# Performance work log

Hardware: AMD Instinct MI355X
Metric: run time of the kernel (lower is better)

Reference implementation:

```python
import jax, jax.numpy as jnp
import numpy as np

B, N, C, H, D = 1, 256, 128, 4, 32  # batch, n_res, c_z, heads, head_dim
LN_EPS = 1e-5


def setup_inputs() -> dict:
    key = jax.random.key(0)
    ks = jax.random.split(key, 10)
    s = 0.02
    return {
        "act": jax.random.normal(ks[0], (B, N, N, C), dtype=jnp.float32),
        "mask": jnp.ones((B, N, N), dtype=jnp.float32),
        "ln_g": jnp.ones((C,), dtype=jnp.float32),
        "ln_b": jnp.zeros((C,), dtype=jnp.float32),
        "w2d": jax.random.normal(ks[1], (C, H), dtype=jnp.float32) * s,
        "wq": jax.random.normal(ks[2], (C, H, D), dtype=jnp.float32) * s,
        "wk": jax.random.normal(ks[3], (C, H, D), dtype=jnp.float32) * s,
        "wv": jax.random.normal(ks[4], (C, H, D), dtype=jnp.float32) * s,
        "wg": jax.random.normal(ks[5], (C, H, D), dtype=jnp.float32) * s,
        "bg": jnp.ones((H, D), dtype=jnp.float32),
        "wo": jax.random.normal(ks[6], (H, D, C), dtype=jnp.float32) * s,
        "bo": jnp.zeros((C,), dtype=jnp.float32),
    }


def reference(act, mask, ln_g, ln_b, w2d, wq, wk, wv, wg, bg, wo, bo):
    # LayerNorm over channel dim
    mu = jnp.mean(act, axis=-1, keepdims=True)
    var = jnp.mean(jnp.square(act - mu), axis=-1, keepdims=True)
    x = (act - mu) * jax.lax.rsqrt(var + LN_EPS) * ln_g + ln_b  # [B,N,N,C]

    # mask bias: [B, I, 1, 1, K]
    mask_bias = (1e9 * (mask - 1.0))[:, :, None, None, :]
    # nonbatched pair bias: [B, 1, H, Q, K]
    nb_bias = jnp.einsum('bqkc,ch->bhqk', x, w2d)[:, None]

    scale = 1.0 / jnp.sqrt(jnp.asarray(D, dtype=x.dtype))
    q = jnp.einsum('bijc,chd->bijhd', x, wq) * scale  # [B,I,Q,H,D]
    k = jnp.einsum('bijc,chd->bijhd', x, wk)
    v = jnp.einsum('bijc,chd->bijhd', x, wv)

    logits = jnp.einsum('biqhd,bikhd->bihqk', q, k) + mask_bias + nb_bias
    a = jax.nn.softmax(logits, axis=-1)  # [B,I,H,Q,K]
    o = jnp.einsum('bihqk,bikhd->biqhd', a, v)  # [B,I,Q,H,D]

    g = jax.nn.sigmoid(jnp.einsum('bijc,chd->bijhd', x, wg) + bg)
    o = o * g
    out = jnp.einsum('biqhd,hdc->biqc', o, wo) + bo  # [B,N,N,C]
    return out
```

## Files before the change

kernel.cpp:

```cpp
#include <hip/hip_runtime.h>

#define QK_SCALE 0.17677669529663689f

typedef float f4 __attribute__((ext_vector_type(4)));
typedef short bf16x8 __attribute__((ext_vector_type(8)));
typedef float f32x4 __attribute__((ext_vector_type(4)));
typedef unsigned short us4 __attribute__((ext_vector_type(4)));

__device__ __forceinline__ unsigned short f2bf(float x){
  unsigned int u = __float_as_uint(x);
  u += 0x7fffu + ((u >> 16) & 1u);
  return (unsigned short)(u >> 16);
}
__device__ __forceinline__ float bf2f(unsigned short h){
  return __uint_as_float(((unsigned int)h) << 16);
}
__device__ __forceinline__ f32x4 mfma16(bf16x8 a, bf16x8 b, f32x4 c){
  return __builtin_amdgcn_mfma_f32_16x16x32_bf16(a, b, c, 0, 0, 0);
}
__device__ __forceinline__ void gload_lds16(const void* g, void* s){
  __builtin_amdgcn_global_load_lds(
      (const __attribute__((address_space(1))) unsigned int*)g,
      (__attribute__((address_space(3))) unsigned int*)s, 16, 0, 0);
}

__global__ __launch_bounds__(256)
void k_prep(const float* __restrict__ wq, const float* __restrict__ wk,
            const float* __restrict__ wv, const float* __restrict__ wg,
            const float* __restrict__ wo, unsigned short* __restrict__ pk)
{
  const int m = blockIdx.x;
  const float* W = (m==0)? wq : (m==1)? wk : (m==2)? wv : (m==3)? wg : wo;
  const float scale = (m==0)? QK_SCALE : 1.0f;
  unsigned short* dst = pk + (long)m * 32768;
  for (int ent = threadIdx.x; ent < 2048; ent += 256){
    const int l = ent & 63, ktn = ent >> 6;
    const int kt = ktn & 3, nt = ktn >> 2;
    unsigned short* ph = dst + ((nt*4 + kt)*2 + 0)*512 + l*8;
    unsigned short* pl = dst + ((nt*4 + kt)*2 + 1)*512 + l*8;
    #pragma unroll
    for (int e = 0; e < 8; ++e){
      const int row = kt*32 + (l>>4)*8 + e;
      const int col = nt*16 + (l&15);
      float v = W[row*128 + col] * scale;
      unsigned short hh = f2bf(v);
      ph[e] = hh;
      pl[e] = f2bf(v - bf2f(hh));
    }
  }
}

__global__ __launch_bounds__(512, 2)
void k_proj(const float* __restrict__ act, const float* __restrict__ ln_g,
            const float* __restrict__ ln_b, const float* __restrict__ w2d,
            const unsigned short* __restrict__ pk, const float* __restrict__ bg,
            unsigned short* __restrict__ qf, unsigned short* __restrict__ kf,
            unsigned short* __restrict__ vt, unsigned short* __restrict__ gg,
            float* __restrict__ b2d)
{
  __shared__ float xs[128*132];
  __shared__ unsigned short afr[8*4*2*512];
  __shared__ unsigned short sc[8*640];
  const int t = threadIdx.x, w = t>>6, l = t&63, g16 = l>>4, c = l&15;
  const long p0 = (long)blockIdx.x * 128;
  const int bi = (int)(p0 >> 8);
  const int qb0 = (int)(p0 & 255);

  { const f4* af = (const f4*)(act + p0*128);
    #pragma unroll
    for (int j = 0; j < 8; ++j){
      int fi = t + j*512, r = fi>>5, c4 = (fi&31)<<2;
      *(f4*)&xs[r*132 + c4] = af[fi];
    } }
  __syncthreads();
  {
    const int r = t>>2, sub = t&3;
    float s=0.f, s2=0.f;
    #pragma unroll 8
    for (int jj=0; jj<32; ++jj){ float x = xs[r*132+sub*32+jj]; s+=x; s2+=x*x; }
    s += __shfl_xor(s,1); s2 += __shfl_xor(s2,1);
    s += __shfl_xor(s,2); s2 += __shfl_xor(s2,2);
    const float mu = s*(1.f/128.f);
    const float iv = rsqrtf(fmaxf(s2*(1.f/128.f)-mu*mu,0.f)+1e-5f);
    #pragma unroll 8
    for (int jj=0; jj<32; ++jj){
      int cc = sub*32+jj;
      xs[r*132+cc] = (xs[r*132+cc]-mu)*iv*ln_g[cc]+ln_b[cc];
    } }
  __syncthreads();

  #pragma unroll
  for (int kt = 0; kt < 4; ++kt){
    const float* xp = &xs[(w*16+c)*132 + kt*32 + g16*8];
    f4 x0 = *(const f4*)xp, x1 = *(const f4*)(xp+4);
    bf16x8 hv, lv;
    #pragma unroll
    for (int e = 0; e < 8; ++e){
      float vvv = (e<4)? x0[e] : x1[e-4];
      unsigned short hh = f2bf(vvv);
      hv[e] = (short)hh; lv[e] = (short)f2bf(vvv - bf2f(hh));
    }
    *(bf16x8*)&afr[((w*4+kt)*2+0)*512 + l*8] = hv;
    *(bf16x8*)&afr[((w*4+kt)*2+1)*512 + l*8] = lv;
  }
  {
    const int r = t>>2, hh = t&3;
    float s = 0.f;
    #pragma unroll 8
    for (int cc = 0; cc < 128; ++cc) s += xs[r*132+cc]*w2d[cc*4+hh];
    b2d[hh*65536 + (int)p0 + r] = s;
  }
  __syncthreads();

  unsigned short* scw = sc + w*640;

  #pragma unroll
  for (int pass = 0; pass < 2; ++pass){
    bf16x8 bh0[4], bl0[4], bh1[4], bl1[4];
    { const int ntg = w*4 + pass*2;
      #pragma unroll
      for (int kt = 0; kt < 4; ++kt){
        bh0[kt] = *(const bf16x8*)(pk + ((ntg*4+kt)*2+0)*512 + l*8);
        bl0[kt] = *(const bf16x8*)(pk + ((ntg*4+kt)*2+1)*512 + l*8);
        bh1[kt] = *(const bf16x8*)(pk + (((ntg+1)*4+kt)*2+0)*512 + l*8);
        bl1[kt] = *(const bf16x8*)(pk + (((ntg+1)*4+kt)*2+1)*512 + l*8);
      } }
    for (int rt = 0; rt < 8; ++rt){
      bf16x8 ah[4], al[4];
      #pragma unroll
      for (int kt = 0; kt < 4; ++kt){
        ah[kt] = *(const bf16x8*)&afr[((rt*4+kt)*2+0)*512 + l*8];
        al[kt] = *(const bf16x8*)&afr[((rt*4+kt)*2+1)*512 + l*8];
      }
      f32x4 a0 = {0.f,0.f,0.f,0.f}, a1 = {0.f,0.f,0.f,0.f};
      #pragma unroll
      for (int kt = 0; kt < 4; ++kt){
        a0 = mfma16(ah[kt], bh0[kt], a0);
        a1 = mfma16(ah[kt], bh1[kt], a1);
        a0 = mfma16(ah[kt], bl0[kt], a0);
        a1 = mfma16(ah[kt], bl1[kt], a1);
        a0 = mfma16(al[kt], bh0[kt], a0);
        a1 = mfma16(al[kt], bh1[kt], a1);
      }
      if (w < 4){
        #pragma unroll
        for (int j = 0; j < 4; ++j){
          scw[(g16*4+j)*40 + c]      = f2bf(a0[j]);
          scw[(g16*4+j)*40 + 16 + c] = f2bf(a1[j]);
        }
        asm volatile("" ::: "memory");
        bf16x8 fr = *(const bf16x8*)&scw[c*40 + g16*8];
        const int head = (w&1)*2 + pass;
        unsigned short* dst = (w < 2) ? qf : kf;
        *(bf16x8*)&dst[(((long)bi*4+head)*16 + (qb0>>4) + rt)*512 + l*8] = fr;
        asm volatile("" ::: "memory");
      } else if (w < 6){
        const int ntv0 = (w-4)*4 + pass*2;
        const int kv = qb0 + rt*16 + g16*4;
        #pragma unroll
        for (int np = 0; np < 2; ++np){
          const int colg = (ntv0+np)*16 + c;
          const int head = colg >> 5, d = colg & 31;
          f32x4 aa = np ? a1 : a0;
          us4 v4;
          #pragma unroll
          for (int j = 0; j < 4; ++j) v4[j] = f2bf(aa[j]);
          const int vb = (d*512 + kv*2) ^ ((d&7)<<4);
          *(us4*)((char*)vt + ((long)bi*4+head)*16384 + vb) = v4;
        }
      } else {
        const int colb = (w-6)*64 + pass*32;
        const int row0 = (int)p0 + rt*16 + g16*4;
        const float bg0 = bg[colb + c];
        const float bg1 = bg[colb + 16 + c];
        #pragma unroll
        for (int j = 0; j < 4; ++j){
          float g0 = 1.f/(1.f + __expf(-(a0[j] + bg0)));
          float g1 = 1.f/(1.f + __expf(-(a1[j] + bg1)));
          gg[(row0+j)*128 + colb + c]      = f2bf(g0);
          gg[(row0+j)*128 + colb + 16 + c] = f2bf(g1);
        }
      }
    }
  }
}

__global__ __launch_bounds__(256, 2)
void k_attn(const unsigned short* __restrict__ qf, const unsigned short* __restrict__ kfg,
            const unsigned short* __restrict__ vt, const unsigned short* __restrict__ gg,
            const float* __restrict__ b2d, const float* __restrict__ mask,
            float* __restrict__ o)
{
  __shared__ unsigned short k_s[16*512];
  __shared__ unsigned short v_s[8192];
  __shared__ unsigned short p_s[4*4224];
  __shared__ float mb_s[256];
  const int t = threadIdx.x, w = t>>6, l = t&63, g16 = l>>4, c = l&15;
  const int bi = blockIdx.x >> 2, h = blockIdx.x & 3;
  const int base = (bi*4+h)*8192;

  #pragma unroll
  for (int cc = 0; cc < 8; ++cc){
    const int ch = w*8 + cc;
    if (ch < 16) gload_lds16(kfg + base + ch*512 + l*8, k_s + ch*512);
    else         gload_lds16(vt + base + (ch-16)*512 + l*8, v_s + (ch-16)*512);
  }
  mb_s[t] = 1e9f * (mask[bi*256 + t] - 1.0f);
  asm volatile("s_waitcnt vmcnt(0)" ::: "memory");
  __syncthreads();

  unsigned short* pw = p_s + w*4224;

  for (int im = 0; im < 4; ++im){
    const int q0 = w*64 + im*16;
    const bf16x8 qfr = *(const bf16x8*)(qf + base + (q0>>4)*512 + l*8);
    f32x4 sa[16];
    #pragma unroll
    for (int nt = 0; nt < 16; ++nt){
      const int kcol = nt*16 + c;
      const float mbv = mb_s[kcol];
      const float* bp = b2d + h*65536 + (q0 + g16*4)*256 + kcol;
      f32x4 ci;
      ci[0]=mbv+bp[0]; ci[1]=mbv+bp[256]; ci[2]=mbv+bp[512]; ci[3]=mbv+bp[768];
      sa[nt] = mfma16(qfr, *(const bf16x8*)(k_s + nt*512 + l*8), ci);
    }
    float mx0=-3e38f,mx1=-3e38f,mx2=-3e38f,mx3=-3e38f;
    #pragma unroll
    for (int nt = 0; nt < 16; ++nt){
      mx0 = fmaxf(mx0, sa[nt][0]); mx1 = fmaxf(mx1, sa[nt][1]);
      mx2 = fmaxf(mx2, sa[nt][2]); mx3 = fmaxf(mx3, sa[nt][3]);
    }
    #pragma unroll
    for (int d = 1; d < 16; d <<= 1){
      mx0 = fmaxf(mx0, __shfl_xor(mx0, d)); mx1 = fmaxf(mx1, __shfl_xor(mx1, d));
      mx2 = fmaxf(mx2, __shfl_xor(mx2, d)); mx3 = fmaxf(mx3, __shfl_xor(mx3, d));
    }
    float s0=0.f, s1=0.f, s2=0.f, s3=0.f;
    #pragma unroll
    for (int nt = 0; nt < 16; ++nt){
      float e0 = __expf(sa[nt][0]-mx0), e1 = __expf(sa[nt][1]-mx1);
      float e2 = __expf(sa[nt][2]-mx2), e3 = __expf(sa[nt][3]-mx3);
      s0 += e0; s1 += e1; s2 += e2; s3 += e3;
      const int cb = nt*16 + c;
      pw[(g16*4+0)*264 + cb] = f2bf(e0);
      pw[(g16*4+1)*264 + cb] = f2bf(e1);
      pw[(g16*4+2)*264 + cb] = f2bf(e2);
      pw[(g16*4+3)*264 + cb] = f2bf(e3);
    }
    #pragma unroll
    for (int d = 1; d < 16; d <<= 1){
      s0 += __shfl_xor(s0, d); s1 += __shfl_xor(s1, d);
      s2 += __shfl_xor(s2, d); s3 += __shfl_xor(s3, d);
    }
    float invs[4] = {1.f/s0, 1.f/s1, 1.f/s2, 1.f/s3};
    asm volatile("s_waitcnt lgkmcnt(0)" ::: "memory");
    __builtin_amdgcn_sched_barrier(0);
    f32x4 oa0 = {0.f,0.f,0.f,0.f}, oa1 = {0.f,0.f,0.f,0.f};
    #pragma unroll
    for (int kt = 0; kt < 8; ++kt){
      bf16x8 pf = *(const bf16x8*)(pw + c*264 + kt*32 + g16*8);
      const int vb0 = ((c*512      + kt*64 + g16*16) ^ ((c&7)<<4));
      const int vb1 = (((16+c)*512 + kt*64 + g16*16) ^ ((c&7)<<4));
      oa0 = mfma16(pf, *(const bf16x8*)((const char*)v_s + vb0), oa0);
      oa1 = mfma16(pf, *(const bf16x8*)((const char*)v_s + vb1), oa1);
    }
    const int row0 = bi*256 + q0 + g16*4;
    #pragma unroll
    for (int j = 0; j < 4; ++j){
      float gv0 = bf2f(gg[(row0+j)*128 + h*32 + c]);
      float gv1 = bf2f(gg[(row0+j)*128 + h*32 + 16 + c]);
      o[(row0+j)*128 + h*32 + c]      = oa0[j]*invs[j]*gv0;
      o[(row0+j)*128 + h*32 + 16 + c] = oa1[j]*invs[j]*gv1;
    }
  }
}

__global__ __launch_bounds__(512, 2)
void k_out(const float* __restrict__ oi, const unsigned short* __restrict__ pko,
           const float* __restrict__ bo, float* __restrict__ out)
{
  __shared__ float xs[128*132];
  __shared__ unsigned short afr[8*4*2*512];
  const int t = threadIdx.x, w = t>>6, l = t&63, g16 = l>>4, c = l&15;
  const long p0 = (long)blockIdx.x * 128;

  { const f4* af = (const f4*)(oi + p0*128);
    #pragma unroll
    for (int j = 0; j < 8; ++j){
      int fi = t + j*512, r = fi>>5, c4 = (fi&31)<<2;
      *(f4*)&xs[r*132 + c4] = af[fi];
    } }
  __syncthreads();
  #pragma unroll
  for (int kt = 0; kt < 4; ++kt){
    const float* xp = &xs[(w*16+c)*132 + kt*32 + g16*8];
    f4 x0 = *(const f4*)xp, x1 = *(const f4*)(xp+4);
    bf16x8 hv, lv;
    #pragma unroll
    for (int e = 0; e < 8; ++e){
      float vvv = (e<4)? x0[e] : x1[e-4];
      unsigned short hh = f2bf(vvv);
      hv[e] = (short)hh; lv[e] = (short)f2bf(vvv - bf2f(hh));
    }
    *(bf16x8*)&afr[((w*4+kt)*2+0)*512 + l*8] = hv;
    *(bf16x8*)&afr[((w*4+kt)*2+1)*512 + l*8] = lv;
  }
  __syncthreads();

  bf16x8 bh[4], bl[4];
  #pragma unroll
  for (int kt = 0; kt < 4; ++kt){
    bh[kt] = *(const bf16x8*)(pko + ((w*4+kt)*2+0)*512 + l*8);
    bl[kt] = *(const bf16x8*)(pko + ((w*4+kt)*2+1)*512 + l*8);
  }
  const float bov = bo[w*16 + c];
  for (int rt = 0; rt < 8; ++rt){
    bf16x8 ah[4], al[4];
    #pragma unroll
    for (int kt = 0; kt < 4; ++kt){
      ah[kt] = *(const bf16x8*)&afr[((rt*4+kt)*2+0)*512 + l*8];
      al[kt] = *(const bf16x8*)&afr[((rt*4+kt)*2+1)*512 + l*8];
    }
    f32x4 a0 = {bov, bov, bov, bov};
    #pragma unroll
    for (int kt = 0; kt < 4; ++kt){
      a0 = mfma16(ah[kt], bh[kt], a0);
      a0 = mfma16(ah[kt], bl[kt], a0);
      a0 = mfma16(al[kt], bh[kt], a0);
    }
    const int row0 = (int)p0 + rt*16 + g16*4;
    #pragma unroll
    for (int j = 0; j < 4; ++j)
      out[(row0+j)*128 + w*16 + c] = a0[j];
  }
}

extern "C" void kernel_launch(void* const* d_in, const int* in_sizes, int n_in,
                              void* d_out, int out_size, void* d_ws, size_t ws_size,
                              hipStream_t stream) {
  const float* act  = (const float*)d_in[0];
  const float* mask = (const float*)d_in[1];
  const float* ln_g = (const float*)d_in[2];
  const float* ln_b = (const float*)d_in[3];
  const float* w2d  = (const float*)d_in[4];
  const float* wq   = (const float*)d_in[5];
  const float* wk   = (const float*)d_in[6];
  const float* wv   = (const float*)d_in[7];
  const float* wg   = (const float*)d_in[8];
  const float* bg   = (const float*)d_in[9];
  const float* wo   = (const float*)d_in[10];
  const float* bo   = (const float*)d_in[11];
  float* out = (float*)d_out;

  char* ws = (char*)d_ws;
  unsigned short* qf  = (unsigned short*)(ws);
  unsigned short* kfb = (unsigned short*)(ws + 16777216L);
  unsigned short* vt  = (unsigned short*)(ws + 33554432L);
  unsigned short* gg  = (unsigned short*)(ws + 50331648L);
  float* o   = (float*)(ws + 67108864L);
  float* b2d = (float*)(ws + 100663296L);
  unsigned short* pk = (unsigned short*)(ws + 101711872L);

  k_prep<<<5, 256, 0, stream>>>(wq, wk, wv, wg, wo, pk);
  k_proj<<<512, 512, 0, stream>>>(act, ln_g, ln_b, w2d, pk, bg,
                                  qf, kfb, vt, gg, b2d);
  k_attn<<<1024, 256, 0, stream>>>(qf, kfb, vt, gg, b2d, mask, o);
  k_out<<<512, 512, 0, stream>>>(o, pk + 4*32768, bo, out);
}
```

Before: 127.6 us.

## Register-resident LayerNorm, bf16 attention output, halved P staging, lighter out-projection

k_proj now loads each row straight into registers, computes LayerNorm with cross-lane shuffles and fuses the pair-bias dot product into the split-bf16 pass. This drops the 66KB fp32 LDS staging buffer so more blocks can be resident (launch bounds raised). k_attn writes its gated output as bf16 instead of fp32 and stages P in two halves to halve LDS. It also hoists the bias loads ahead of the QK MFMAs. k_out loads the bf16 activations directly into LDS and does two MFMAs per k-step instead of three, trading output-projection precision (activations no longer hi/lo split) for less traffic and compute.

```diff
diff --git a/kernel.cpp b/kernel.cpp
--- a/kernel.cpp
+++ b/kernel.cpp
@@ -50,7 +50,7 @@
   }
 }
 
-__global__ __launch_bounds__(512, 2)
+__global__ __launch_bounds__(512, 4)
 void k_proj(const float* __restrict__ act, const float* __restrict__ ln_g,
             const float* __restrict__ ln_b, const float* __restrict__ w2d,
             const unsigned short* __restrict__ pk, const float* __restrict__ bg,
@@ -58,61 +58,66 @@
             unsigned short* __restrict__ vt, unsigned short* __restrict__ gg,
             float* __restrict__ b2d)
 {
-  __shared__ float xs[128*132];
   __shared__ unsigned short afr[8*4*2*512];
-  __shared__ unsigned short sc[8*640];
+  __shared__ unsigned short sc[4*640];
   const int t = threadIdx.x, w = t>>6, l = t&63, g16 = l>>4, c = l&15;
   const long p0 = (long)blockIdx.x * 128;
   const int bi = (int)(p0 >> 8);
   const int qb0 = (int)(p0 & 255);
-
-  { const f4* af = (const f4*)(act + p0*128);
-    #pragma unroll
-    for (int j = 0; j < 8; ++j){
-      int fi = t + j*512, r = fi>>5, c4 = (fi&31)<<2;
-      *(f4*)&xs[r*132 + c4] = af[fi];
-    } }
-  __syncthreads();
+  const int row = w*16 + c;
+
   {
-    const int r = t>>2, sub = t&3;
-    float s=0.f, s2=0.f;
-    #pragma unroll 8
-    for (int jj=0; jj<32; ++jj){ float x = xs[r*132+sub*32+jj]; s+=x; s2+=x*x; }
-    s += __shfl_xor(s,1); s2 += __shfl_xor(s2,1);
-    s += __shfl_xor(s,2); s2 += __shfl_xor(s2,2);
+    const float* ap = act + (p0 + row)*128;
+    f4 xv[4][2];
+    #pragma unroll
+    for (int kt = 0; kt < 4; ++kt){
+      xv[kt][0] = *(const f4*)(ap + kt*32 + g16*8);
+      xv[kt][1] = *(const f4*)(ap + kt*32 + g16*8 + 4);
+    }
+    float s = 0.f, s2 = 0.f;
+    #pragma unroll
+    for (int kt = 0; kt < 4; ++kt)
+      #pragma unroll
+      for (int u = 0; u < 2; ++u)
+        #pragma unroll
+        for (int e = 0; e < 4; ++e){
+          float x = xv[kt][u][e]; s += x; s2 += x*x;
+        }
+    s += __shfl_xor(s,16); s2 += __shfl_xor(s2,16);
+    s += __shfl_xor(s,32); s2 += __shfl_xor(s2,32);
     const float mu = s*(1.f/128.f);
     const float iv = rsqrtf(fmaxf(s2*(1.f/128.f)-mu*mu,0.f)+1e-5f);
-    #pragma unroll 8
-    for (int jj=0; jj<32; ++jj){
-      int cc = sub*32+jj;
-      xs[r*132+cc] = (xs[r*132+cc]-mu)*iv*ln_g[cc]+ln_b[cc];
-    } }
+
+    float pb0=0.f, pb1=0.f, pb2=0.f, pb3=0.f;
+    #pragma unroll
+    for (int kt = 0; kt < 4; ++kt){
+      bf16x8 hv, lv;
+      #pragma unroll
+      for (int u = 0; u < 2; ++u){
+        const int cb = kt*32 + g16*8 + u*4;
+        f4 lg = *(const f4*)(ln_g + cb);
+        f4 lb = *(const f4*)(ln_b + cb);
+        #pragma unroll
+        for (int e0 = 0; e0 < 4; ++e0){
+          float vv = (xv[kt][u][e0]-mu)*iv*lg[e0] + lb[e0];
+          f4 wp = *(const f4*)(w2d + (cb+e0)*4);
+          pb0 += vv*wp[0]; pb1 += vv*wp[1]; pb2 += vv*wp[2]; pb3 += vv*wp[3];
+          unsigned short hh = f2bf(vv);
+          hv[u*4+e0] = (short)hh;
+          lv[u*4+e0] = (short)f2bf(vv - bf2f(hh));
+        }
+      }
+      *(bf16x8*)&afr[((w*4+kt)*2+0)*512 + l*8] = hv;
+      *(bf16x8*)&afr[((w*4+kt)*2+1)*512 + l*8] = lv;
+    }
+    pb0 += __shfl_xor(pb0,16); pb1 += __shfl_xor(pb1,16);
+    pb2 += __shfl_xor(pb2,16); pb3 += __shfl_xor(pb3,16);
+    pb0 += __shfl_xor(pb0,32); pb1 += __shfl_xor(pb1,32);
+    pb2 += __shfl_xor(pb2,32); pb3 += __shfl_xor(pb3,32);
+    const float pbsel = (g16==0)? pb0 : (g16==1)? pb1 : (g16==2)? pb2 : pb3;
+    b2d[g16*65536 + (int)p0 + row] = pbsel;
+  }
   __syncthreads();
-
-  #pragma unroll
-  for (int kt = 0; kt < 4; ++kt){
-    const float* xp = &xs[(w*16+c)*132 + kt*32 + g16*8];
-    f4 x0 = *(const f4*)xp, x1 = *(const f4*)(xp+4);
-    bf16x8 hv, lv;
-    #pragma unroll
-    for (int e = 0; e < 8; ++e){
-      float vvv = (e<4)? x0[e] : x1[e-4];
-      unsigned short hh = f2bf(vvv);
-      hv[e] = (short)hh; lv[e] = (short)f2bf(vvv - bf2f(hh));
-    }
-    *(bf16x8*)&afr[((w*4+kt)*2+0)*512 + l*8] = hv;
-    *(bf16x8*)&afr[((w*4+kt)*2+1)*512 + l*8] = lv;
-  }
-  {
-    const int r = t>>2, hh = t&3;
-    float s = 0.f;
-    #pragma unroll 8
-    for (int cc = 0; cc < 128; ++cc) s += xs[r*132+cc]*w2d[cc*4+hh];
-    b2d[hh*65536 + (int)p0 + r] = s;
-  }
-  __syncthreads();
-
-  unsigned short* scw = sc + w*640;
 
   #pragma unroll
   for (int pass = 0; pass < 2; ++pass){
@@ -143,6 +148,7 @@
         a1 = mfma16(al[kt], bh1[kt], a1);
       }
       if (w < 4){
+        unsigned short* scw = sc + w*640;
         #pragma unroll
         for (int j = 0; j < 4; ++j){
           scw[(g16*4+j)*40 + c]      = f2bf(a0[j]);
@@ -185,15 +191,15 @@
   }
 }
 
-__global__ __launch_bounds__(256, 2)
+__global__ __launch_bounds__(256, 3)
 void k_attn(const unsigned short* __restrict__ qf, const unsigned short* __restrict__ kfg,
             const unsigned short* __restrict__ vt, const unsigned short* __restrict__ gg,
             const float* __restrict__ b2d, const float* __restrict__ mask,
-            float* __restrict__ o)
+            unsigned short* __restrict__ obf)
 {
   __shared__ unsigned short k_s[16*512];
   __shared__ unsigned short v_s[8192];
-  __shared__ unsigned short p_s[4*4224];
+  __shared__ unsigned short p_s[4*2112];
   __shared__ float mb_s[256];
   const int t = threadIdx.x, w = t>>6, l = t&63, g16 = l>>4, c = l&15;
   const int bi = blockIdx.x >> 2, h = blockIdx.x & 3;
@@ -209,21 +215,25 @@
   asm volatile("s_waitcnt vmcnt(0)" ::: "memory");
   __syncthreads();
 
-  unsigned short* pw = p_s + w*4224;
+  unsigned short* pw = p_s + w*2112;
 
   for (int im = 0; im < 4; ++im){
     const int q0 = w*64 + im*16;
     const bf16x8 qfr = *(const bf16x8*)(qf + base + (q0>>4)*512 + l*8);
     f32x4 sa[16];
+    const float* bq = b2d + h*65536 + (q0 + g16*4)*256;
     #pragma unroll
     for (int nt = 0; nt < 16; ++nt){
       const int kcol = nt*16 + c;
       const float mbv = mb_s[kcol];
-      const float* bp = b2d + h*65536 + (q0 + g16*4)*256 + kcol;
       f32x4 ci;
-      ci[0]=mbv+bp[0]; ci[1]=mbv+bp[256]; ci[2]=mbv+bp[512]; ci[3]=mbv+bp[768];
-      sa[nt] = mfma16(qfr, *(const bf16x8*)(k_s + nt*512 + l*8), ci);
-    }
+      ci[0]=mbv+bq[kcol];     ci[1]=mbv+bq[256+kcol];
+      ci[2]=mbv+bq[512+kcol]; ci[3]=mbv+bq[768+kcol];
+      sa[nt] = ci;
+    }
+    #pragma unroll
+    for (int nt = 0; nt < 16; ++nt)
+      sa[nt] = mfma16(qfr, *(const bf16x8*)(k_s + nt*512 + l*8), sa[nt]);
     float mx0=-3e38f,mx1=-3e38f,mx2=-3e38f,mx3=-3e38f;
     #pragma unroll
     for (int nt = 0; nt < 16; ++nt){
@@ -241,11 +251,7 @@
       float e0 = __expf(sa[nt][0]-mx0), e1 = __expf(sa[nt][1]-mx1);
       float e2 = __expf(sa[nt][2]-mx2), e3 = __expf(sa[nt][3]-mx3);
       s0 += e0; s1 += e1; s2 += e2; s3 += e3;
-      const int cb = nt*16 + c;
-      pw[(g16*4+0)*264 + cb] = f2bf(e0);
-      pw[(g16*4+1)*264 + cb] = f2bf(e1);
-      pw[(g16*4+2)*264 + cb] = f2bf(e2);
-      pw[(g16*4+3)*264 + cb] = f2bf(e3);
+      sa[nt][0]=e0; sa[nt][1]=e1; sa[nt][2]=e2; sa[nt][3]=e3;
     }
     #pragma unroll
     for (int d = 1; d < 16; d <<= 1){
@@ -253,58 +259,58 @@
       s2 += __shfl_xor(s2, d); s3 += __shfl_xor(s3, d);
     }
     float invs[4] = {1.f/s0, 1.f/s1, 1.f/s2, 1.f/s3};
-    asm volatile("s_waitcnt lgkmcnt(0)" ::: "memory");
-    __builtin_amdgcn_sched_barrier(0);
     f32x4 oa0 = {0.f,0.f,0.f,0.f}, oa1 = {0.f,0.f,0.f,0.f};
     #pragma unroll
-    for (int kt = 0; kt < 8; ++kt){
-      bf16x8 pf = *(const bf16x8*)(pw + c*264 + kt*32 + g16*8);
-      const int vb0 = ((c*512      + kt*64 + g16*16) ^ ((c&7)<<4));
-      const int vb1 = (((16+c)*512 + kt*64 + g16*16) ^ ((c&7)<<4));
-      oa0 = mfma16(pf, *(const bf16x8*)((const char*)v_s + vb0), oa0);
-      oa1 = mfma16(pf, *(const bf16x8*)((const char*)v_s + vb1), oa1);
+    for (int ph = 0; ph < 2; ++ph){
+      #pragma unroll
+      for (int n8 = 0; n8 < 8; ++n8){
+        const int nt = ph*8 + n8;
+        const int cb = n8*16 + c;
+        pw[(g16*4+0)*132 + cb] = f2bf(sa[nt][0]);
+        pw[(g16*4+1)*132 + cb] = f2bf(sa[nt][1]);
+        pw[(g16*4+2)*132 + cb] = f2bf(sa[nt][2]);
+        pw[(g16*4+3)*132 + cb] = f2bf(sa[nt][3]);
+      }
+      asm volatile("s_waitcnt lgkmcnt(0)" ::: "memory");
+      __builtin_amdgcn_sched_barrier(0);
+      #pragma unroll
+      for (int ktl = 0; ktl < 4; ++ktl){
+        const int kt = ph*4 + ktl;
+        bf16x8 pf = *(const bf16x8*)(pw + c*132 + ktl*32 + g16*8);
+        const int vb0 = ((c*512      + kt*64 + g16*16) ^ ((c&7)<<4));
+        const int vb1 = (((16+c)*512 + kt*64 + g16*16) ^ ((c&7)<<4));
+        oa0 = mfma16(pf, *(const bf16x8*)((const char*)v_s + vb0), oa0);
+        oa1 = mfma16(pf, *(const bf16x8*)((const char*)v_s + vb1), oa1);
+      }
+      asm volatile("" ::: "memory");
+      __builtin_amdgcn_sched_barrier(0);
     }
     const int row0 = bi*256 + q0 + g16*4;
     #pragma unroll
     for (int j = 0; j < 4; ++j){
       float gv0 = bf2f(gg[(row0+j)*128 + h*32 + c]);
       float gv1 = bf2f(gg[(row0+j)*128 + h*32 + 16 + c]);
-      o[(row0+j)*128 + h*32 + c]      = oa0[j]*invs[j]*gv0;
-      o[(row0+j)*128 + h*32 + 16 + c] = oa1[j]*invs[j]*gv1;
-    }
-  }
-}
-
-__global__ __launch_bounds__(512, 2)
-void k_out(const float* __restrict__ oi, const unsigned short* __restrict__ pko,
+      obf[(row0+j)*128 + h*32 + c]      = f2bf(oa0[j]*invs[j]*gv0);
+      obf[(row0+j)*128 + h*32 + 16 + c] = f2bf(oa1[j]*invs[j]*gv1);
+    }
+  }
+}
+
+__global__ __launch_bounds__(512, 4)
+void k_out(const unsigned short* __restrict__ obf, const unsigned short* __restrict__ pko,
            const float* __restrict__ bo, float* __restrict__ out)
 {
-  __shared__ float xs[128*132];
-  __shared__ unsigned short afr[8*4*2*512];
+  __shared__ unsigned short afr[32*512];
   const int t = threadIdx.x, w = t>>6, l = t&63, g16 = l>>4, c = l&15;
   const long p0 = (long)blockIdx.x * 128;
 
-  { const f4* af = (const f4*)(oi + p0*128);
-    #pragma unroll
-    for (int j = 0; j < 8; ++j){
-      int fi = t + j*512, r = fi>>5, c4 = (fi&31)<<2;
-      *(f4*)&xs[r*132 + c4] = af[fi];
-    } }
-  __syncthreads();
   #pragma unroll
-  for (int kt = 0; kt < 4; ++kt){
-    const float* xp = &xs[(w*16+c)*132 + kt*32 + g16*8];
-    f4 x0 = *(const f4*)xp, x1 = *(const f4*)(xp+4);
-    bf16x8 hv, lv;
-    #pragma unroll
-    for (int e = 0; e < 8; ++e){
-      float vvv = (e<4)? x0[e] : x1[e-4];
-      unsigned short hh = f2bf(vvv);
-      hv[e] = (short)hh; lv[e] = (short)f2bf(vvv - bf2f(hh));
-    }
-    *(bf16x8*)&afr[((w*4+kt)*2+0)*512 + l*8] = hv;
-    *(bf16x8*)&afr[((w*4+kt)*2+1)*512 + l*8] = lv;
-  }
+  for (int u = 0; u < 4; ++u){
+    const int pr = w*4 + u;
+    const int rt = pr >> 2, kt = pr & 3;
+    gload_lds16(obf + (p0 + rt*16 + c)*128 + kt*32 + g16*8, afr + pr*512);
+  }
+  asm volatile("s_waitcnt vmcnt(0)" ::: "memory");
   __syncthreads();
 
   bf16x8 bh[4], bl[4];
@@ -315,18 +321,12 @@
   }
   const float bov = bo[w*16 + c];
   for (int rt = 0; rt < 8; ++rt){
-    bf16x8 ah[4], al[4];
+    f32x4 a0 = {bov, bov, bov, bov};
     #pragma unroll
     for (int kt = 0; kt < 4; ++kt){
-      ah[kt] = *(const bf16x8*)&afr[((rt*4+kt)*2+0)*512 + l*8];
-      al[kt] = *(const bf16x8*)&afr[((rt*4+kt)*2+1)*512 + l*8];
-    }
-    f32x4 a0 = {bov, bov, bov, bov};
-    #pragma unroll
-    for (int kt = 0; kt < 4; ++kt){
-      a0 = mfma16(ah[kt], bh[kt], a0);
-      a0 = mfma16(ah[kt], bl[kt], a0);
-      a0 = mfma16(al[kt], bh[kt], a0);
+      bf16x8 af = *(const bf16x8*)&afr[(rt*4+kt)*512 + l*8];
+      a0 = mfma16(af, bh[kt], a0);
+      a0 = mfma16(af, bl[kt], a0);
     }
     const int row0 = (int)p0 + rt*16 + g16*4;
     #pragma unroll
@@ -357,13 +357,13 @@
   unsigned short* kfb = (unsigned short*)(ws + 16777216L);
   unsigned short* vt  = (unsigned short*)(ws + 33554432L);
   unsigned short* gg  = (unsigned short*)(ws + 50331648L);
-  float* o   = (float*)(ws + 67108864L);
-  float* b2d = (float*)(ws + 100663296L);
-  unsigned short* pk = (unsigned short*)(ws + 101711872L);
+  unsigned short* obf = (unsigned short*)(ws + 67108864L);
+  float* b2d = (float*)(ws + 83886080L);
+  unsigned short* pk = (unsigned short*)(ws + 84934656L);
 
   k_prep<<<5, 256, 0, stream>>>(wq, wk, wv, wg, wo, pk);
   k_proj<<<512, 512, 0, stream>>>(act, ln_g, ln_b, w2d, pk, bg,
                                   qf, kfb, vt, gg, b2d);
-  k_attn<<<1024, 256, 0, stream>>>(qf, kfb, vt, gg, b2d, mask, o);
-  k_out<<<512, 512, 0, stream>>>(o, pk + 4*32768, bo, out);
-}
+  k_attn<<<1024, 256, 0, stream>>>(qf, kfb, vt, gg, b2d, mask, obf);
+  k_out<<<512, 512, 0, stream>>>(obf, pk + 4*32768, bo, out);
+}
```

Result: faster. 108.3 us (-15.1%).
